# Kernel optimization log

Hardware: AMD Instinct MI355X
Metric: run time of the kernel (lower is better)

## Reference

```python
import jax, jax.numpy as jnp
import numpy as np

NUM_HEADS = 12
N_TOKENS = 1

def setup_inputs() -> dict:
    key = jax.random.key(0)
    ks = jax.random.split(key, 13)
    D = 768
    s = 0.02
    return {
        "x": jax.random.normal(ks[0], (64, 1025, D), jnp.float32),
        "qW": jax.random.normal(ks[1], (D, D), jnp.float32) * s,
        "qb": jax.random.normal(ks[2], (D,), jnp.float32) * s,
        "kW": jax.random.normal(ks[3], (D, D), jnp.float32) * s,
        "kb": jax.random.normal(ks[4], (D,), jnp.float32) * s,
        "vW": jax.random.normal(ks[5], (D, D), jnp.float32) * s,
        "vb": jax.random.normal(ks[6], (D,), jnp.float32) * s,
        "w1W": jax.random.normal(ks[7], (NUM_HEADS, NUM_HEADS), jnp.float32) * 0.1,
        "w1b": jax.random.normal(ks[8], (NUM_HEADS,), jnp.float32) * 0.1,
        "w2W": jax.random.normal(ks[9], (NUM_HEADS, NUM_HEADS), jnp.float32) * 0.1,
        "w2b": jax.random.normal(ks[10], (NUM_HEADS,), jnp.float32) * 0.1,
        "projW": jax.random.normal(ks[11], (D, D), jnp.float32) * s,
        "projb": jax.random.normal(ks[12], (D,), jnp.float32) * s,
    }

def reference(x, qW, qb, kW, kb, vW, vb, w1W, w1b, w2W, w2b, projW, projb):
    B, N, C = x.shape  # C == embed_dim == 768
    H = NUM_HEADS
    d = C // H
    scale = d ** -0.5
    cls = x[:, :N_TOKENS]  # [B, n, C]
    # torch Linear: y = x @ W.T + b
    q = (cls @ qW.T + qb).reshape(B, N_TOKENS, H, d).transpose(0, 2, 1, 3) * scale  # [B,H,n,d]
    k = (x @ kW.T + kb).reshape(B, N, H, d).transpose(0, 2, 1, 3)  # [B,H,N,d]
    v = (x @ vW.T + vb).reshape(B, N, H, d).transpose(0, 2, 1, 3)  # [B,H,N,d]
    attn = jnp.einsum('bhqd,bhkd->bhqk', q, k)  # [B,H,n,N]
    # talking-heads pre-softmax: linear over head dim, added residually
    attn = attn + jnp.einsum('bhqk,gh->bgqk', attn, w1W) + w1b[None, :, None, None]
    attn = jax.nn.softmax(attn, axis=-1)
    # talking-heads post-softmax
    attn = attn + jnp.einsum('bhqk,gh->bgqk', attn, w2W) + w2b[None, :, None, None]
    out = jnp.einsum('bhqk,bhkd->bhqd', attn, v)  # [B,H,n,d]
    out = out.transpose(0, 2, 1, 3).reshape(B, N_TOKENS, C)
    return out @ projW.T + projb
```

## Files before the change

### kernel.cpp

```cpp
#include <hip/hip_runtime.h>

#define B 64
#define N 1025
#define C 768
#define H 12
#define HD 64
#define NT 17

__device__ __forceinline__ float wave_reduce_add(float v) {
    #pragma unroll
    for (int m = 1; m < 64; m <<= 1) v += __shfl_xor(v, m, 64);
    return v;
}

__global__ __launch_bounds__(256) void k_qproj(const float* __restrict__ x,
                                               const float* __restrict__ qW,
                                               const float* __restrict__ qb,
                                               float* __restrict__ qout) {
    __shared__ float cls[4 * C];
    int bt = blockIdx.x, ct = blockIdx.y, tid = threadIdx.x;
    for (int i = tid; i < 768; i += 256) {
        int bl = i / 192, c4 = i % 192;
        ((float4*)cls)[i] = ((const float4*)(x + (size_t)(bt * 4 + bl) * N * C))[c4];
    }
    __syncthreads();
    int w = tid >> 6, lane = tid & 63;
    int b = bt * 4 + w;
    const float* clsrow = &cls[w * C];
    for (int cl = 0; cl < 16; ++cl) {
        int c = ct * 16 + cl;
        const float4* wr = (const float4*)(qW + (size_t)c * C + lane * 12);
        const float4* xr = (const float4*)(clsrow + lane * 12);
        float acc = 0.f;
        #pragma unroll
        for (int s = 0; s < 3; ++s) {
            float4 a = wr[s], v = xr[s];
            acc += a.x * v.x + a.y * v.y + a.z * v.z + a.w * v.w;
        }
        acc = wave_reduce_add(acc);
        if (lane == 0) qout[b * C + c] = 0.125f * (acc + qb[c]);
    }
}

__global__ __launch_bounds__(256) void k_qk(const float* __restrict__ q,
                                            const float* __restrict__ kW,
                                            const float* __restrict__ kb,
                                            float* __restrict__ qk,
                                            float* __restrict__ qkb) {
    int bt = blockIdx.x, h = blockIdx.y, tid = threadIdx.x;
    if (tid < 192) {
        float4 acc[4] = {};
        #pragma unroll 4
        for (int i = 0; i < HD; ++i) {
            int row = h * HD + i;
            float4 kv = *(const float4*)(kW + (size_t)row * C + tid * 4);
            #pragma unroll
            for (int bl = 0; bl < 4; ++bl) {
                float qv = q[(bt * 4 + bl) * C + row];
                acc[bl].x += qv * kv.x; acc[bl].y += qv * kv.y;
                acc[bl].z += qv * kv.z; acc[bl].w += qv * kv.w;
            }
        }
        #pragma unroll
        for (int bl = 0; bl < 4; ++bl) {
            int b = bt * 4 + bl;
            *(float4*)(qk + ((size_t)b * H + h) * C + tid * 4) = acc[bl];
        }
    }
    int w = tid >> 6, lane = tid & 63;
    int b = bt * 4 + w;
    float v = q[b * C + h * HD + lane] * kb[h * HD + lane];
    v = wave_reduce_add(v);
    if (lane == 0) qkb[b * H + h] = v;
}

__global__ __launch_bounds__(256) void k_scores(const float* __restrict__ x,
                                                const float* __restrict__ qk,
                                                const float* __restrict__ qkbias,
                                                const float* __restrict__ w1W,
                                                const float* __restrict__ w1b,
                                                float* __restrict__ sc,
                                                float* __restrict__ mstat,
                                                float* __restrict__ sstat) {
    __shared__ float qs[12 * C];
    __shared__ float w1s[144], w1bs[12], qbs[12];
    int tile = blockIdx.x, b = blockIdx.y, tid = threadIdx.x;
    const float4* qksrc = (const float4*)(qk + (size_t)b * H * C);
    for (int i = tid; i < 2304; i += 256) ((float4*)qs)[i] = qksrc[i];
    if (tid < 144) w1s[tid] = w1W[tid];
    if (tid < 12)  { w1bs[tid] = w1b[tid]; qbs[tid] = qkbias[b * 12 + tid]; }
    __syncthreads();
    int w = tid >> 6, lane = tid & 63;
    int c16 = lane & 15, r = lane >> 4;
    int rowbase = tile * 64 + w * 16 + r * 4;
    const float* xb = x + (size_t)b * N * C;
    float acc[4][12] = {};
    for (int cc = 0; cc < C; cc += 128) {
        int c0 = cc + c16 * 4, c1 = c0 + 64;
        float4 xv0[4], xv1[4];
        #pragma unroll
        for (int j = 0; j < 4; ++j) {
            int row = rowbase + j;
            const float* xr = xb + (size_t)row * C;
            xv0[j] = (row < N) ? *(const float4*)(xr + c0) : make_float4(0.f,0.f,0.f,0.f);
            xv1[j] = (row < N) ? *(const float4*)(xr + c1) : make_float4(0.f,0.f,0.f,0.f);
        }
        #pragma unroll
        for (int h = 0; h < 12; ++h) {
            float4 q0 = *(const float4*)(qs + h * C + c0);
            float4 q1 = *(const float4*)(qs + h * C + c1);
            #pragma unroll
            for (int j = 0; j < 4; ++j) {
                acc[j][h] += xv0[j].x * q0.x + xv0[j].y * q0.y +
                             xv0[j].z * q0.z + xv0[j].w * q0.w;
                acc[j][h] += xv1[j].x * q1.x + xv1[j].y * q1.y +
                             xv1[j].z * q1.z + xv1[j].w * q1.w;
            }
        }
    }
    #pragma unroll
    for (int j = 0; j < 4; ++j)
        #pragma unroll
        for (int h = 0; h < 12; ++h) {
            float v = acc[j][h];
            v += __shfl_xor(v, 1); v += __shfl_xor(v, 2);
            v += __shfl_xor(v, 4); v += __shfl_xor(v, 8);
            acc[j][h] = v;
        }
    __syncthreads();
    if (c16 == 0) {
        #pragma unroll
        for (int j = 0; j < 4; ++j)
            #pragma unroll
            for (int h = 0; h < 12; ++h)
                qs[(w * 16 + r * 4 + j) * 12 + h] = acc[j][h];
    }
    __syncthreads();
    if (tid < 64) {
        int row = tile * 64 + tid;
        bool valid = row < N;
        float s_[12], o[12];
        #pragma unroll
        for (int h = 0; h < 12; ++h) s_[h] = qs[tid * 12 + h] + qbs[h];
        #pragma unroll
        for (int g = 0; g < 12; ++g) {
            float a = s_[g] + w1bs[g];
            #pragma unroll
            for (int h = 0; h < 12; ++h) a += w1s[g * 12 + h] * s_[h];
            o[g] = a;
        }
        if (valid) {
            float* sp = sc + ((size_t)b * N + row) * 12;
            *(float4*)(sp)     = make_float4(o[0], o[1], o[2],  o[3]);
            *(float4*)(sp + 4) = make_float4(o[4], o[5], o[6],  o[7]);
            *(float4*)(sp + 8) = make_float4(o[8], o[9], o[10], o[11]);
        }
        #pragma unroll
        for (int g = 0; g < 12; ++g) {
            float mv = valid ? o[g] : -3e38f;
            #pragma unroll
            for (int m = 1; m < 64; m <<= 1) mv = fmaxf(mv, __shfl_xor(mv, m, 64));
            float e = valid ? __expf(o[g] - mv) : 0.f;
            e = wave_reduce_add(e);
            if (tid == 0) {
                mstat[((size_t)b * NT + tile) * 12 + g] = mv;
                sstat[((size_t)b * NT + tile) * 12 + g] = e;
            }
        }
    }
}

#define FMA4(d, s, xv) { d.x += (s) * xv.x; d.y += (s) * xv.y; d.z += (s) * xv.z; d.w += (s) * xv.w; }
__global__ __launch_bounds__(384) void k_ysum(const float* __restrict__ x,
                                              const float* __restrict__ sc,
                                              const float* __restrict__ mstat,
                                              const float* __restrict__ sstat,
                                              const float* __restrict__ w2W,
                                              const float* __restrict__ w2b,
                                              float* __restrict__ yp) {
    __shared__ float as_[129 * 12];
    __shared__ float4 redv[192 * 12];
    __shared__ float w2s[144], w2bs[12], msh[12], ish[12];
    int k = blockIdx.x, b = blockIdx.y, tid = threadIdx.x;
    int nlo = k * 128, nn = (k == 7) ? 129 : 128;
    if (tid < 144) w2s[tid] = w2W[tid];
    if (tid < 12) {
        w2bs[tid] = w2b[tid];
        float m = -3e38f, mv[NT];
        #pragma unroll
        for (int kk = 0; kk < NT; ++kk) {
            mv[kk] = mstat[((size_t)b * NT + kk) * 12 + tid];
            m = fmaxf(m, mv[kk]);
        }
        float S = 0.f;
        #pragma unroll
        for (int kk = 0; kk < NT; ++kk)
            S += sstat[((size_t)b * NT + kk) * 12 + tid] * __expf(mv[kk] - m);
        msh[tid] = m; ish[tid] = 1.f / S;
    }
    __syncthreads();
    if (tid < nn) {
        int n = nlo + tid;
        const float* sp = sc + ((size_t)b * N + n) * 12;
        float4 s0 = *(const float4*)(sp);
        float4 s1 = *(const float4*)(sp + 4);
        float4 s2 = *(const float4*)(sp + 8);
        float p[12];
        p[0]  = __expf(s0.x - msh[0])  * ish[0];
        p[1]  = __expf(s0.y - msh[1])  * ish[1];
        p[2]  = __expf(s0.z - msh[2])  * ish[2];
        p[3]  = __expf(s0.w - msh[3])  * ish[3];
        p[4]  = __expf(s1.x - msh[4])  * ish[4];
        p[5]  = __expf(s1.y - msh[5])  * ish[5];
        p[6]  = __expf(s1.z - msh[6])  * ish[6];
        p[7]  = __expf(s1.w - msh[7])  * ish[7];
        p[8]  = __expf(s2.x - msh[8])  * ish[8];
        p[9]  = __expf(s2.y - msh[9])  * ish[9];
        p[10] = __expf(s2.z - msh[10]) * ish[10];
        p[11] = __expf(s2.w - msh[11]) * ish[11];
        #pragma unroll
        for (int g = 0; g < 12; ++g) {
            float a = p[g] + w2bs[g];
            #pragma unroll
            for (int h = 0; h < 12; ++h) a += w2s[g * 12 + h] * p[h];
            as_[tid * 12 + g] = a;
        }
    }
    __syncthreads();
    int grp = tid / 192, t = tid - grp * 192;
    int n0   = grp ? 64 : 0;
    int nend = grp ? nn : 64;
    const float* xb = x + ((size_t)b * N + nlo) * C + t * 4;
    float4 acc[12] = {};
    int n = n0;
    for (; n + 4 <= nend; n += 4) {
        float4 xv[4];
        #pragma unroll
        for (int u = 0; u < 4; ++u)
            xv[u] = *(const float4*)(xb + (size_t)(n + u) * C);
        #pragma unroll
        for (int u = 0; u < 4; ++u) {
            const float4* ar = (const float4*)(as_ + (n + u) * 12);
            float4 a0 = ar[0], a1 = ar[1], a2 = ar[2];
            FMA4(acc[0], a0.x, xv[u]); FMA4(acc[1], a0.y, xv[u]); FMA4(acc[2], a0.z, xv[u]); FMA4(acc[3], a0.w, xv[u]);
            FMA4(acc[4], a1.x, xv[u]); FMA4(acc[5], a1.y, xv[u]); FMA4(acc[6], a1.z, xv[u]); FMA4(acc[7], a1.w, xv[u]);
            FMA4(acc[8], a2.x, xv[u]); FMA4(acc[9], a2.y, xv[u]); FMA4(acc[10], a2.z, xv[u]); FMA4(acc[11], a2.w, xv[u]);
        }
    }
    for (; n < nend; ++n) {
        float4 xv = *(const float4*)(xb + (size_t)n * C);
        const float4* ar = (const float4*)(as_ + n * 12);
        float4 a0 = ar[0], a1 = ar[1], a2 = ar[2];
        FMA4(acc[0], a0.x, xv); FMA4(acc[1], a0.y, xv); FMA4(acc[2], a0.z, xv); FMA4(acc[3], a0.w, xv);
        FMA4(acc[4], a1.x, xv); FMA4(acc[5], a1.y, xv); FMA4(acc[6], a1.z, xv); FMA4(acc[7], a1.w, xv);
        FMA4(acc[8], a2.x, xv); FMA4(acc[9], a2.y, xv); FMA4(acc[10], a2.z, xv); FMA4(acc[11], a2.w, xv);
    }
    if (grp == 1) {
        #pragma unroll
        for (int h = 0; h < 12; ++h) redv[t * 12 + h] = acc[h];
    }
    __syncthreads();
    if (grp == 0) {
        #pragma unroll
        for (int h = 0; h < 12; ++h) {
            float4 rv = redv[t * 12 + h];
            acc[h].x += rv.x; acc[h].y += rv.y; acc[h].z += rv.z; acc[h].w += rv.w;
        }
        #pragma unroll
        for (int h = 0; h < 12; ++h)
            *(float4*)(yp + (((size_t)k * B + b) * H + h) * C + t * 4) = acc[h];
    }
}

__global__ __launch_bounds__(256) void k_zproj(const float* __restrict__ yp,
                                               const float* __restrict__ vW,
                                               const float* __restrict__ vb,
                                               const float* __restrict__ w2W,
                                               const float* __restrict__ w2b,
                                               float* __restrict__ z) {
    __shared__ float ys[4 * C];
    int bt = blockIdx.x, h = blockIdx.y, tid = threadIdx.x;
    for (int i = tid; i < 768; i += 256) {
        int bl = i / 192, c4 = i % 192;
        int b = bt * 4 + bl;
        float4 s = make_float4(0.f, 0.f, 0.f, 0.f);
        #pragma unroll
        for (int k = 0; k < 8; ++k) {
            float4 v = ((const float4*)(yp + (((size_t)k * B + b) * H + h) * C))[c4];
            s.x += v.x; s.y += v.y; s.z += v.z; s.w += v.w;
        }
        ((float4*)ys)[i] = s;
    }
    __syncthreads();
    float sv = 1.f + 1025.f * w2b[h];
    #pragma unroll
    for (int j = 0; j < 12; ++j) sv += w2W[h * 12 + j];
    int w = tid >> 6, lane = tid & 63;
    int b = bt * 4 + w;
    const float* yrow = &ys[w * C];
    for (int cl = 0; cl < 64; ++cl) {
        int c = h * 64 + cl;
        const float4* wr = (const float4*)(vW + (size_t)c * C + lane * 12);
        const float4* yr = (const float4*)(yrow + lane * 12);
        float acc = 0.f;
        #pragma unroll
        for (int s = 0; s < 3; ++s) {
            float4 a = wr[s], v = yr[s];
            acc += a.x * v.x + a.y * v.y + a.z * v.z + a.w * v.w;
        }
        acc = wave_reduce_add(acc);
        if (lane == 0) z[b * C + c] = acc + vb[c] * sv;
    }
}

__global__ __launch_bounds__(256) void k_out(const float* __restrict__ z,
                                             const float* __restrict__ pW,
                                             const float* __restrict__ pb,
                                             float* __restrict__ out) {
    __shared__ float zs[4 * C];
    int bt = blockIdx.x, ct = blockIdx.y, tid = threadIdx.x;
    for (int i = tid; i < 768; i += 256)
        ((float4*)zs)[i] = ((const float4*)(z + (size_t)bt * 4 * C))[i];
    __syncthreads();
    int w = tid >> 6, lane = tid & 63;
    int b = bt * 4 + w;
    for (int cl = 0; cl < 16; ++cl) {
        int c = ct * 16 + cl;
        const float4* wr = (const float4*)(pW + (size_t)c * C + lane * 12);
        const float4* zr = (const float4*)(zs + w * C + lane * 12);
        float acc = 0.f;
        #pragma unroll
        for (int s = 0; s < 3; ++s) {
            float4 a = wr[s], v = zr[s];
            acc += a.x * v.x + a.y * v.y + a.z * v.z + a.w * v.w;
        }
        acc = wave_reduce_add(acc);
        if (lane == 0) out[b * C + c] = acc + pb[c];
    }
}

extern "C" void kernel_launch(void* const* d_in, const int* in_sizes, int n_in,
                              void* d_out, int out_size, void* d_ws, size_t ws_size,
                              hipStream_t stream) {
    const float* x    = (const float*)d_in[0];
    const float* qW   = (const float*)d_in[1];
    const float* qb   = (const float*)d_in[2];
    const float* kW   = (const float*)d_in[3];
    const float* kb   = (const float*)d_in[4];
    const float* vW   = (const float*)d_in[5];
    const float* vb   = (const float*)d_in[6];
    const float* w1W  = (const float*)d_in[7];
    const float* w1b  = (const float*)d_in[8];
    const float* w2W  = (const float*)d_in[9];
    const float* w2b  = (const float*)d_in[10];
    const float* pW   = (const float*)d_in[11];
    const float* pb   = (const float*)d_in[12];
    float* out = (float*)d_out;

    float* ws    = (float*)d_ws;
    float* qk    = ws + 0;
    float* qkb   = ws + 589824;
    float* q     = ws + 590592;
    float* sc    = ws + 639744;
    float* yp    = ws + 1426944;
    float* z     = ws + 6145536;
    float* mstat = ws + 6194688;
    float* sstat = ws + 6207744;

    k_qproj <<<dim3(16, 48), 256, 0, stream>>>(x, qW, qb, q);
    k_qk    <<<dim3(16, 12), 256, 0, stream>>>(q, kW, kb, qk, qkb);
    k_scores<<<dim3(17, 64), 256, 0, stream>>>(x, qk, qkb, w1W, w1b, sc, mstat, sstat);
    k_ysum  <<<dim3(8, 64), 384, 0, stream>>>(x, sc, mstat, sstat, w2W, w2b, yp);
    k_zproj <<<dim3(16, 12), 256, 0, stream>>>(yp, vW, vb, w2W, w2b, z);
    k_out   <<<dim3(16, 48), 256, 0, stream>>>(z, pW, pb, out);
}
```

Measured before the change: 454.9 us.

## Fuse scores with weighted x-sum per tile and drop max-subtraction softmax

The score kernel now also computes exp(scores) and the per-tile weighted sum of x rows while the tile is still hot in cache. This removes the separate pass that re-read all of x and the score buffer. Per-tile partial sums are written in bf16, and a new combine kernel normalises them and applies the post-softmax head mixing, with the bias term handled through a plain x-sum. The running-max subtraction is dropped, which risks overflow for large scores, and the bf16 partials lower precision. The x loads in the score loop are also software-prefetched one chunk ahead.

```diff
diff --git a/kernel.cpp b/kernel.cpp
--- a/kernel.cpp
+++ b/kernel.cpp
@@ -1,11 +1,12 @@
 #include <hip/hip_runtime.h>
+#include <hip/hip_bf16.h>
 
 #define B 64
 #define N 1025
 #define C 768
 #define H 12
 #define HD 64
-#define NT 17
+#define TILES 17
 
 __device__ __forceinline__ float wave_reduce_add(float v) {
     #pragma unroll
@@ -74,14 +75,14 @@
     if (lane == 0) qkb[b * H + h] = v;
 }
 
-__global__ __launch_bounds__(256) void k_scores(const float* __restrict__ x,
-                                                const float* __restrict__ qk,
-                                                const float* __restrict__ qkbias,
-                                                const float* __restrict__ w1W,
-                                                const float* __restrict__ w1b,
-                                                float* __restrict__ sc,
-                                                float* __restrict__ mstat,
-                                                float* __restrict__ sstat) {
+__global__ __launch_bounds__(256) void k_att(const float* __restrict__ x,
+                                             const float* __restrict__ qk,
+                                             const float* __restrict__ qkbias,
+                                             const float* __restrict__ w1W,
+                                             const float* __restrict__ w1b,
+                                             __hip_bfloat16* __restrict__ ype,
+                                             float* __restrict__ ypx,
+                                             float* __restrict__ sstat) {
     __shared__ float qs[12 * C];
     __shared__ float w1s[144], w1bs[12], qbs[12];
     int tile = blockIdx.x, b = blockIdx.y, tid = threadIdx.x;
@@ -89,33 +90,43 @@
     for (int i = tid; i < 2304; i += 256) ((float4*)qs)[i] = qksrc[i];
     if (tid < 144) w1s[tid] = w1W[tid];
     if (tid < 12)  { w1bs[tid] = w1b[tid]; qbs[tid] = qkbias[b * 12 + tid]; }
-    __syncthreads();
-    int w = tid >> 6, lane = tid & 63;
+
+    int lane = tid & 63, w = tid >> 6;
     int c16 = lane & 15, r = lane >> 4;
     int rowbase = tile * 64 + w * 16 + r * 4;
     const float* xb = x + (size_t)b * N * C;
+    const float4 z4 = make_float4(0.f, 0.f, 0.f, 0.f);
+
+    float4 xcur[4], xnxt[4];
+    #pragma unroll
+    for (int j = 0; j < 4; ++j) {
+        int row = rowbase + j;
+        xcur[j] = (row < N) ? *(const float4*)(xb + (size_t)row * C + c16 * 4) : z4;
+    }
+    __syncthreads();
+
     float acc[4][12] = {};
-    for (int cc = 0; cc < C; cc += 128) {
-        int c0 = cc + c16 * 4, c1 = c0 + 64;
-        float4 xv0[4], xv1[4];
-        #pragma unroll
-        for (int j = 0; j < 4; ++j) {
-            int row = rowbase + j;
-            const float* xr = xb + (size_t)row * C;
-            xv0[j] = (row < N) ? *(const float4*)(xr + c0) : make_float4(0.f,0.f,0.f,0.f);
-            xv1[j] = (row < N) ? *(const float4*)(xr + c1) : make_float4(0.f,0.f,0.f,0.f);
-        }
+    for (int cc = 0; cc < 12; ++cc) {
+        if (cc < 11) {
+            int cn = (cc + 1) * 64 + c16 * 4;
+            #pragma unroll
+            for (int j = 0; j < 4; ++j) {
+                int row = rowbase + j;
+                xnxt[j] = (row < N) ? *(const float4*)(xb + (size_t)row * C + cn) : z4;
+            }
+        }
+        int cq = cc * 64 + c16 * 4;
         #pragma unroll
         for (int h = 0; h < 12; ++h) {
-            float4 q0 = *(const float4*)(qs + h * C + c0);
-            float4 q1 = *(const float4*)(qs + h * C + c1);
-            #pragma unroll
-            for (int j = 0; j < 4; ++j) {
-                acc[j][h] += xv0[j].x * q0.x + xv0[j].y * q0.y +
-                             xv0[j].z * q0.z + xv0[j].w * q0.w;
-                acc[j][h] += xv1[j].x * q1.x + xv1[j].y * q1.y +
-                             xv1[j].z * q1.z + xv1[j].w * q1.w;
-            }
+            float4 q0 = *(const float4*)(qs + h * C + cq);
+            #pragma unroll
+            for (int j = 0; j < 4; ++j)
+                acc[j][h] += xcur[j].x * q0.x + xcur[j].y * q0.y +
+                             xcur[j].z * q0.z + xcur[j].w * q0.w;
+        }
+        if (cc < 11) {
+            #pragma unroll
+            for (int j = 0; j < 4; ++j) xcur[j] = xnxt[j];
         }
     }
     #pragma unroll
@@ -139,7 +150,7 @@
     if (tid < 64) {
         int row = tile * 64 + tid;
         bool valid = row < N;
-        float s_[12], o[12];
+        float s_[12], e[12];
         #pragma unroll
         for (int h = 0; h < 12; ++h) s_[h] = qs[tid * 12 + h] + qbs[h];
         #pragma unroll
@@ -147,132 +158,96 @@
             float a = s_[g] + w1bs[g];
             #pragma unroll
             for (int h = 0; h < 12; ++h) a += w1s[g * 12 + h] * s_[h];
-            o[g] = a;
-        }
-        if (valid) {
-            float* sp = sc + ((size_t)b * N + row) * 12;
-            *(float4*)(sp)     = make_float4(o[0], o[1], o[2],  o[3]);
-            *(float4*)(sp + 4) = make_float4(o[4], o[5], o[6],  o[7]);
-            *(float4*)(sp + 8) = make_float4(o[8], o[9], o[10], o[11]);
-        }
+            e[g] = valid ? __expf(a) : 0.f;
+        }
+        #pragma unroll
+        for (int g = 0; g < 12; ++g) qs[tid * 12 + g] = e[g];
         #pragma unroll
         for (int g = 0; g < 12; ++g) {
-            float mv = valid ? o[g] : -3e38f;
-            #pragma unroll
-            for (int m = 1; m < 64; m <<= 1) mv = fmaxf(mv, __shfl_xor(mv, m, 64));
-            float e = valid ? __expf(o[g] - mv) : 0.f;
-            e = wave_reduce_add(e);
-            if (tid == 0) {
-                mstat[((size_t)b * NT + tile) * 12 + g] = mv;
-                sstat[((size_t)b * NT + tile) * 12 + g] = e;
+            float sg = wave_reduce_add(e[g]);
+            if (tid == 0) sstat[((size_t)b * TILES + tile) * 12 + g] = sg;
+        }
+    }
+    __syncthreads();
+
+    float pacc[12][3] = {};
+    float xs[3] = {0.f, 0.f, 0.f};
+    int nv = N - tile * 64; if (nv > 64) nv = 64;
+    for (int n0 = 0; n0 < 64; n0 += 4) {
+        float xv[4][3];
+        #pragma unroll
+        for (int u = 0; u < 4; ++u) {
+            int n = n0 + u;
+            const float* xr = xb + (size_t)(tile * 64 + n) * C + tid;
+            bool val = n < nv;
+            xv[u][0] = val ? xr[0]   : 0.f;
+            xv[u][1] = val ? xr[256] : 0.f;
+            xv[u][2] = val ? xr[512] : 0.f;
+        }
+        #pragma unroll
+        for (int u = 0; u < 4; ++u) {
+            const float* er = qs + (n0 + u) * 12;
+            xs[0] += xv[u][0]; xs[1] += xv[u][1]; xs[2] += xv[u][2];
+            #pragma unroll
+            for (int h = 0; h < 12; ++h) {
+                float ev = er[h];
+                pacc[h][0] += ev * xv[u][0];
+                pacc[h][1] += ev * xv[u][1];
+                pacc[h][2] += ev * xv[u][2];
             }
         }
     }
-}
-
-#define FMA4(d, s, xv) { d.x += (s) * xv.x; d.y += (s) * xv.y; d.z += (s) * xv.z; d.w += (s) * xv.w; }
-__global__ __launch_bounds__(384) void k_ysum(const float* __restrict__ x,
-                                              const float* __restrict__ sc,
-                                              const float* __restrict__ mstat,
-                                              const float* __restrict__ sstat,
-                                              const float* __restrict__ w2W,
-                                              const float* __restrict__ w2b,
-                                              float* __restrict__ yp) {
-    __shared__ float as_[129 * 12];
-    __shared__ float4 redv[192 * 12];
-    __shared__ float w2s[144], w2bs[12], msh[12], ish[12];
-    int k = blockIdx.x, b = blockIdx.y, tid = threadIdx.x;
-    int nlo = k * 128, nn = (k == 7) ? 129 : 128;
+    size_t base = (size_t)tile * B + b;
+    #pragma unroll
+    for (int h = 0; h < 12; ++h) {
+        __hip_bfloat16* dst = ype + (base * 12 + h) * C + tid;
+        dst[0]   = __float2bfloat16(pacc[h][0]);
+        dst[256] = __float2bfloat16(pacc[h][1]);
+        dst[512] = __float2bfloat16(pacc[h][2]);
+    }
+    float* xdst = ypx + base * C + tid;
+    xdst[0] = xs[0]; xdst[256] = xs[1]; xdst[512] = xs[2];
+}
+
+__global__ __launch_bounds__(256) void k_combine(const __hip_bfloat16* __restrict__ ype,
+                                                 const float* __restrict__ ypx,
+                                                 const float* __restrict__ sstat,
+                                                 const float* __restrict__ w2W,
+                                                 const float* __restrict__ w2b,
+                                                 float* __restrict__ ybar) {
+    __shared__ float w2s[144], w2bs[12], ish[12];
+    int cg = blockIdx.x, b = blockIdx.y, tid = threadIdx.x;
     if (tid < 144) w2s[tid] = w2W[tid];
     if (tid < 12) {
         w2bs[tid] = w2b[tid];
-        float m = -3e38f, mv[NT];
-        #pragma unroll
-        for (int kk = 0; kk < NT; ++kk) {
-            mv[kk] = mstat[((size_t)b * NT + kk) * 12 + tid];
-            m = fmaxf(m, mv[kk]);
-        }
         float S = 0.f;
         #pragma unroll
-        for (int kk = 0; kk < NT; ++kk)
-            S += sstat[((size_t)b * NT + kk) * 12 + tid] * __expf(mv[kk] - m);
-        msh[tid] = m; ish[tid] = 1.f / S;
-    }
-    __syncthreads();
-    if (tid < nn) {
-        int n = nlo + tid;
-        const float* sp = sc + ((size_t)b * N + n) * 12;
-        float4 s0 = *(const float4*)(sp);
-        float4 s1 = *(const float4*)(sp + 4);
-        float4 s2 = *(const float4*)(sp + 8);
-        float p[12];
-        p[0]  = __expf(s0.x - msh[0])  * ish[0];
-        p[1]  = __expf(s0.y - msh[1])  * ish[1];
-        p[2]  = __expf(s0.z - msh[2])  * ish[2];
-        p[3]  = __expf(s0.w - msh[3])  * ish[3];
-        p[4]  = __expf(s1.x - msh[4])  * ish[4];
-        p[5]  = __expf(s1.y - msh[5])  * ish[5];
-        p[6]  = __expf(s1.z - msh[6])  * ish[6];
-        p[7]  = __expf(s1.w - msh[7])  * ish[7];
-        p[8]  = __expf(s2.x - msh[8])  * ish[8];
-        p[9]  = __expf(s2.y - msh[9])  * ish[9];
-        p[10] = __expf(s2.z - msh[10]) * ish[10];
-        p[11] = __expf(s2.w - msh[11]) * ish[11];
-        #pragma unroll
-        for (int g = 0; g < 12; ++g) {
-            float a = p[g] + w2bs[g];
-            #pragma unroll
-            for (int h = 0; h < 12; ++h) a += w2s[g * 12 + h] * p[h];
-            as_[tid * 12 + g] = a;
-        }
-    }
-    __syncthreads();
-    int grp = tid / 192, t = tid - grp * 192;
-    int n0   = grp ? 64 : 0;
-    int nend = grp ? nn : 64;
-    const float* xb = x + ((size_t)b * N + nlo) * C + t * 4;
-    float4 acc[12] = {};
-    int n = n0;
-    for (; n + 4 <= nend; n += 4) {
-        float4 xv[4];
-        #pragma unroll
-        for (int u = 0; u < 4; ++u)
-            xv[u] = *(const float4*)(xb + (size_t)(n + u) * C);
-        #pragma unroll
-        for (int u = 0; u < 4; ++u) {
-            const float4* ar = (const float4*)(as_ + (n + u) * 12);
-            float4 a0 = ar[0], a1 = ar[1], a2 = ar[2];
-            FMA4(acc[0], a0.x, xv[u]); FMA4(acc[1], a0.y, xv[u]); FMA4(acc[2], a0.z, xv[u]); FMA4(acc[3], a0.w, xv[u]);
-            FMA4(acc[4], a1.x, xv[u]); FMA4(acc[5], a1.y, xv[u]); FMA4(acc[6], a1.z, xv[u]); FMA4(acc[7], a1.w, xv[u]);
-            FMA4(acc[8], a2.x, xv[u]); FMA4(acc[9], a2.y, xv[u]); FMA4(acc[10], a2.z, xv[u]); FMA4(acc[11], a2.w, xv[u]);
-        }
-    }
-    for (; n < nend; ++n) {
-        float4 xv = *(const float4*)(xb + (size_t)n * C);
-        const float4* ar = (const float4*)(as_ + n * 12);
-        float4 a0 = ar[0], a1 = ar[1], a2 = ar[2];
-        FMA4(acc[0], a0.x, xv); FMA4(acc[1], a0.y, xv); FMA4(acc[2], a0.z, xv); FMA4(acc[3], a0.w, xv);
-        FMA4(acc[4], a1.x, xv); FMA4(acc[5], a1.y, xv); FMA4(acc[6], a1.z, xv); FMA4(acc[7], a1.w, xv);
-        FMA4(acc[8], a2.x, xv); FMA4(acc[9], a2.y, xv); FMA4(acc[10], a2.z, xv); FMA4(acc[11], a2.w, xv);
-    }
-    if (grp == 1) {
-        #pragma unroll
-        for (int h = 0; h < 12; ++h) redv[t * 12 + h] = acc[h];
-    }
-    __syncthreads();
-    if (grp == 0) {
-        #pragma unroll
-        for (int h = 0; h < 12; ++h) {
-            float4 rv = redv[t * 12 + h];
-            acc[h].x += rv.x; acc[h].y += rv.y; acc[h].z += rv.z; acc[h].w += rv.w;
-        }
-        #pragma unroll
-        for (int h = 0; h < 12; ++h)
-            *(float4*)(yp + (((size_t)k * B + b) * H + h) * C + t * 4) = acc[h];
-    }
-}
-
-__global__ __launch_bounds__(256) void k_zproj(const float* __restrict__ yp,
+        for (int t = 0; t < TILES; ++t) S += sstat[((size_t)b * TILES + t) * 12 + tid];
+        ish[tid] = 1.f / S;
+    }
+    __syncthreads();
+    int c = cg * 256 + tid;
+    float P[12] = {};
+    float X = 0.f;
+    for (int t = 0; t < TILES; ++t) {
+        size_t base = (size_t)t * B + b;
+        const __hip_bfloat16* src = ype + base * 12 * C + c;
+        #pragma unroll
+        for (int h = 0; h < 12; ++h) P[h] += __bfloat162float(src[h * C]);
+        X += ypx[base * C + c];
+    }
+    #pragma unroll
+    for (int h = 0; h < 12; ++h) P[h] *= ish[h];
+    #pragma unroll
+    for (int g = 0; g < 12; ++g) {
+        float a = P[g] + w2bs[g] * X;
+        #pragma unroll
+        for (int h = 0; h < 12; ++h) a += w2s[g * 12 + h] * P[h];
+        ybar[((size_t)b * 12 + g) * C + c] = a;
+    }
+}
+
+__global__ __launch_bounds__(256) void k_zproj(const float* __restrict__ ybar,
                                                const float* __restrict__ vW,
                                                const float* __restrict__ vb,
                                                const float* __restrict__ w2W,
@@ -283,13 +258,7 @@
     for (int i = tid; i < 768; i += 256) {
         int bl = i / 192, c4 = i % 192;
         int b = bt * 4 + bl;
-        float4 s = make_float4(0.f, 0.f, 0.f, 0.f);
-        #pragma unroll
-        for (int k = 0; k < 8; ++k) {
-            float4 v = ((const float4*)(yp + (((size_t)k * B + b) * H + h) * C))[c4];
-            s.x += v.x; s.y += v.y; s.z += v.z; s.w += v.w;
-        }
-        ((float4*)ys)[i] = s;
+        ((float4*)ys)[i] = ((const float4*)(ybar + ((size_t)b * 12 + h) * C))[c4];
     }
     __syncthreads();
     float sv = 1.f + 1025.f * w2b[h];
@@ -361,16 +330,16 @@
     float* qk    = ws + 0;
     float* qkb   = ws + 589824;
     float* q     = ws + 590592;
-    float* sc    = ws + 639744;
-    float* yp    = ws + 1426944;
-    float* z     = ws + 6145536;
-    float* mstat = ws + 6194688;
-    float* sstat = ws + 6207744;
-
-    k_qproj <<<dim3(16, 48), 256, 0, stream>>>(x, qW, qb, q);
-    k_qk    <<<dim3(16, 12), 256, 0, stream>>>(q, kW, kb, qk, qkb);
-    k_scores<<<dim3(17, 64), 256, 0, stream>>>(x, qk, qkb, w1W, w1b, sc, mstat, sstat);
-    k_ysum  <<<dim3(8, 64), 384, 0, stream>>>(x, sc, mstat, sstat, w2W, w2b, yp);
-    k_zproj <<<dim3(16, 12), 256, 0, stream>>>(yp, vW, vb, w2W, w2b, z);
-    k_out   <<<dim3(16, 48), 256, 0, stream>>>(z, pW, pb, out);
-}
+    float* sstat = ws + 639744;
+    float* ypx   = ws + 652800;
+    __hip_bfloat16* ype = (__hip_bfloat16*)(ws + 1488384);
+    float* ybar  = qk;
+    float* z     = q;
+
+    k_qproj  <<<dim3(16, 48), 256, 0, stream>>>(x, qW, qb, q);
+    k_qk     <<<dim3(16, 12), 256, 0, stream>>>(q, kW, kb, qk, qkb);
+    k_att    <<<dim3(17, 64), 256, 0, stream>>>(x, qk, qkb, w1W, w1b, ype, ypx, sstat);
+    k_combine<<<dim3(3, 64),  256, 0, stream>>>(ype, ypx, sstat, w2W, w2b, ybar);
+    k_zproj  <<<dim3(16, 12), 256, 0, stream>>>(ybar, vW, vb, w2W, w2b, z);
+    k_out    <<<dim3(16, 48), 256, 0, stream>>>(z, pW, pb, out);
+}
```

Result: slower. 498.5 us (+9.6%).
